# Kernel optimization log

Hardware: AMD Instinct MI355X
Metric: run time of the kernel (lower is better)

## Reference

```python
import jax, jax.numpy as jnp
import numpy as np

N = 50000      # total packed nodes
E = 1600000    # edges (no self loops; layers add them)
G = 64         # graphs in the batch
F_IN = 24      # raw node feature dim
D = 64         # hidden dim
H = 4          # attention heads
C = D // H     # 16 channels per head
L = 3          # GAT layers
NEG = 0.2      # LeakyReLU negative slope (GATv2 default)
EPS = 1e-5     # LayerNorm eps


def setup_inputs() -> dict:
    key = jax.random.key(0)
    ks = jax.random.split(key, 16)
    x = jax.random.normal(ks[0], (N, F_IN), jnp.float32)
    src = jax.random.randint(ks[1], (E,), 0, N)
    dst = jax.random.randint(ks[2], (E,), 0, N)
    dst = jnp.where(dst == src, (dst + 1) % N, dst)  # keep edge list self-loop free
    edge_index = jnp.stack([src, dst]).astype(jnp.int32)
    batch = jnp.sort(jax.random.randint(ks[3], (N,), 0, G)).astype(jnp.int32)
    s = 0.1
    return dict(
        x=x, edge_index=edge_index, batch=batch,
        w_in=jax.random.normal(ks[4], (F_IN, D), jnp.float32) * s,
        b_in=jnp.zeros((D,), jnp.float32),
        w_l=jax.random.normal(ks[5], (L, D, D), jnp.float32) * s,
        b_l=jnp.zeros((L, D), jnp.float32),
        w_r=jax.random.normal(ks[6], (L, D, D), jnp.float32) * s,
        b_r=jnp.zeros((L, D), jnp.float32),
        att=jax.random.normal(ks[7], (L, H, C), jnp.float32) * s,
        b_gat=jnp.zeros((L, D), jnp.float32),
        ln_g=jnp.ones((L, D), jnp.float32),
        ln_b=jnp.zeros((L, D), jnp.float32),
        w_g1=jax.random.normal(ks[8], (D, D // 2), jnp.float32) * s,
        b_g1=jnp.zeros((D // 2,), jnp.float32),
        w_g2=jax.random.normal(ks[9], (D // 2, 1), jnp.float32) * s,
        b_g2=jnp.zeros((1,), jnp.float32),
        w_out=jax.random.normal(ks[10], (D, D), jnp.float32) * s,
        b_out=jnp.zeros((D,), jnp.float32),
    )


def _layernorm(h, g, b):
    m = h.mean(-1, keepdims=True)
    v = ((h - m) ** 2).mean(-1, keepdims=True)
    return (h - m) * jax.lax.rsqrt(v + EPS) * g + b


def _gatv2(h, src, dst, wl, bl, wr, br, att, bg):
    n = h.shape[0]
    xl = (h @ wl + bl).reshape(n, H, C)   # source transform
    xr = (h @ wr + br).reshape(n, H, C)   # target transform
    # edge scores: att . leaky_relu(xl[j] + xr[i])  -> [E', H]
    e = jnp.sum(jax.nn.leaky_relu(xl[src] + xr[dst], NEG) * att, axis=-1)
    emax = jax.ops.segment_max(e, dst, num_segments=n)
    ex = jnp.exp(e - emax[dst])
    denom = jax.ops.segment_sum(ex, dst, num_segments=n)
    alpha = ex / denom[dst]               # segment softmax over incoming edges
    out = jax.ops.segment_sum(alpha[:, :, None] * xl[src], dst, num_segments=n)
    return out.reshape(n, D) + bg


def reference(x, edge_index, batch, w_in, b_in, w_l, b_l, w_r, b_r, att, b_gat,
              ln_g, ln_b, w_g1, b_g1, w_g2, b_g2, w_out, b_out):
    n = x.shape[0]
    loops = jnp.arange(n, dtype=edge_index.dtype)
    src = jnp.concatenate([edge_index[0], loops])  # add self loops once
    dst = jnp.concatenate([edge_index[1], loops])
    h = jax.nn.relu(x @ w_in + b_in)
    for i in range(L):
        res = h
        h = _gatv2(h, src, dst, w_l[i], b_l[i], w_r[i], b_r[i], att[i], b_gat[i])
        h = _layernorm(h + res, ln_g[i], ln_b[i])
        if i < L - 1:
            h = jax.nn.relu(h)
    # GlobalAttention pooling: gate MLP -> per-graph softmax -> weighted sum
    gate = jax.nn.relu(h @ w_g1 + b_g1) @ w_g2 + b_g2  # [N, 1]
    gmax = jax.ops.segment_max(gate, batch, num_segments=G)
    ge = jnp.exp(gate - gmax[batch])
    gs = jax.ops.segment_sum(ge, batch, num_segments=G)
    a = ge / jnp.where(gs > 0, gs, 1.0)[batch]
    emb = jax.ops.segment_sum(a * h, batch, num_segments=G)  # [G, D]
    return jax.nn.relu(emb @ w_out + b_out)
```

## Files before the change

### kernel.cpp

```cpp
#include <hip/hip_runtime.h>

#define NEGS   0.2f
#define LN_EPS 1e-5f
#define BSH    7
#define BN     128
#define TILE   4096
#define LOG2E  1.44269504f

typedef const float* __restrict__ fp;
typedef _Float16 v2h __attribute__((ext_vector_type(2)));
typedef _Float16 v8h __attribute__((ext_vector_type(8)));
typedef float    v4f __attribute__((ext_vector_type(4)));

__device__ __forceinline__ v2h u2h(unsigned u){ union{unsigned u; v2h h;} c; c.u = u; return c.h; }
__device__ __forceinline__ unsigned h2u(v2h h){ union{v2h h; unsigned u;} c; c.h = h; return c.u; }

template<int CTRL>
__device__ __forceinline__ float dppadd(float x){
  int y = __builtin_amdgcn_update_dpp(0, __float_as_int(x), CTRL, 0xF, 0xF, true);
  return x + __int_as_float(y);
}
__device__ __forceinline__ float hsum8(float s){
  s = dppadd<0xB1>(s);
  s = dppadd<0x4E>(s);
  s = dppadd<0x141>(s);
  return s;
}
__device__ __forceinline__ float edge_w(v2h v, v2h xrv, v2h att2, float negm8){
  v2h t = v + xrv;
  t = __builtin_elementwise_max(t, t * (_Float16)NEGS);
  float s = hsum8(__builtin_amdgcn_fdot2(t, att2, negm8, false));
  return __builtin_amdgcn_exp2f(s);
}

__global__ __launch_bounds__(256) void k_in(fp x, fp w, fp b, float* __restrict__ h,
                                            unsigned* __restrict__ h16, int N){
  __shared__ float ws[24*64];
  __shared__ float bs[64];
  __shared__ float xs[4][24];
  int tid = threadIdx.x;
  for (int i = tid; i < 24*64; i += 256) ws[i] = w[i];
  if (tid < 64) bs[tid] = b[tid];
  int r = tid >> 6, c = tid & 63;
  int row = blockIdx.x*4 + r;
  if (c < 24 && row < N) xs[r][c] = x[row*24 + c];
  __syncthreads();
  float acc = bs[c];
  #pragma unroll
  for (int k = 0; k < 24; ++k) acc = fmaf(xs[r][k], ws[k*64 + c], acc);
  float y = fmaxf(acc, 0.f);
  float y1 = __shfl_down(y, 1);
  if (row < N){
    h[(size_t)row*64 + c] = y;
    if (!(c & 1)){
      v2h p; p.x = (_Float16)y; p.y = (_Float16)y1;
      h16[(size_t)row*32 + (c >> 1)] = h2u(p);
    }
  }
}

__global__ __launch_bounds__(256) void k_wprep(fp w_l, fp w_r, _Float16* __restrict__ wf){
  int lm = blockIdx.x;
  const float* src = ((lm & 1) ? w_r : w_l) + (lm >> 1)*4096;
  _Float16* dst = wf + lm*4096;
  for (int d = threadIdx.x; d < 4096; d += 256){
    int j = d & 7, l = (d >> 3) & 63, kc = (d >> 9) & 1, nt = d >> 10;
    int k = kc*32 + (l >> 4)*8 + j;
    int n = nt*16 + (l & 15);
    dst[d] = (_Float16)src[k*64 + n];
  }
}

__global__ __launch_bounds__(256) void t_hist(const int* __restrict__ dstA, int* __restrict__ counts,
                                              int E, int K, int ntiles){
  __shared__ int hist[512];
  int t = blockIdx.x, tid = threadIdx.x;
  for (int i = tid; i < K; i += 256) hist[i] = 0;
  __syncthreads();
  int e0 = t*TILE, e1 = min(e0 + TILE, E);
  for (int e = e0 + tid; e < e1; e += 256)
    atomicAdd(&hist[dstA[e] >> BSH], 1);
  __syncthreads();
  for (int i = tid; i < K; i += 256) counts[i*ntiles + t] = hist[i];
}

__global__ __launch_bounds__(512) void s_scan_tiles(int* __restrict__ counts, int* __restrict__ btotal,
                                                    int ntiles){
  __shared__ int s[512];
  int b = blockIdx.x, tid = threadIdx.x;
  int v = (tid < ntiles) ? counts[b*ntiles + tid] : 0;
  s[tid] = v;
  __syncthreads();
  for (int off = 1; off < 512; off <<= 1){
    int t = (tid >= off) ? s[tid - off] : 0;
    __syncthreads();
    s[tid] += t;
    __syncthreads();
  }
  if (tid < ntiles) counts[b*ntiles + tid] = s[tid] - v;
  if (tid == 511) btotal[b] = s[511];
}

__global__ __launch_bounds__(512) void s_scan_buckets(const int* __restrict__ btotal,
                                                      int* __restrict__ bbase, int K, int E){
  __shared__ int s[512];
  int tid = threadIdx.x;
  int v = (tid < K) ? btotal[tid] : 0;
  s[tid] = v;
  __syncthreads();
  for (int off = 1; off < 512; off <<= 1){
    int t = (tid >= off) ? s[tid - off] : 0;
    __syncthreads();
    s[tid] += t;
    __syncthreads();
  }
  if (tid < K) bbase[tid] = s[tid] - v;
  if (tid == 0) bbase[K] = E;
}

__global__ __launch_bounds__(256) void t_scatter(const int* __restrict__ srcA, const int* __restrict__ dstA,
                                                 const int* __restrict__ counts, const int* __restrict__ bbase,
                                                 unsigned* __restrict__ packed, int E, int K, int ntiles){
  __shared__ int gb[512];
  __shared__ int cur[512];
  int t = blockIdx.x, tid = threadIdx.x;
  for (int i = tid; i < K; i += 256){
    gb[i] = bbase[i] + counts[i*ntiles + t];
    cur[i] = 0;
  }
  __syncthreads();
  int e0 = t*TILE, e1 = min(e0 + TILE, E);
  for (int e = e0 + tid; e < e1; e += 256){
    int d = dstA[e], sv = srcA[e];
    int b = d >> BSH;
    int p = atomicAdd(&cur[b], 1);
    packed[gb[b] + p] = ((unsigned)(d & (BN-1)) << 25) | (unsigned)sv;
  }
}

__global__ __launch_bounds__(256) void k_fine(const unsigned* __restrict__ packed, const int* __restrict__ bbase,
                                              int* __restrict__ row_ptr, int* __restrict__ col, int N, int K){
  __shared__ int hist[BN];
  __shared__ int excl[BN];
  int b = blockIdx.x, tid = threadIdx.x;
  int node0 = b << BSH;
  int e_base = bbase[b], e_end = bbase[b+1];
  if (tid < BN) hist[tid] = 0;
  __syncthreads();
  for (int e = e_base + tid; e < e_end; e += 256)
    atomicAdd(&hist[packed[e] >> 25], 1);
  __syncthreads();
  int v = (tid < BN) ? hist[tid] : 0;
  if (tid < BN) excl[tid] = v;
  __syncthreads();
  for (int off = 1; off < BN; off <<= 1){
    int t2 = 0;
    if (tid < BN && tid >= off) t2 = excl[tid - off];
    __syncthreads();
    if (tid < BN) excl[tid] += t2;
    __syncthreads();
  }
  int nn = min(BN, N - node0);
  if (tid < nn) row_ptr[node0 + tid] = e_base + excl[tid] - v;
  if (b == K-1 && tid == 0) row_ptr[N] = e_end;
  if (tid < BN) hist[tid] = excl[tid] - v;
  __syncthreads();
  for (int e = e_base + tid; e < e_end; e += 256){
    unsigned u = packed[e];
    int dl = u >> 25;
    int p = atomicAdd(&hist[dl], 1);
    col[e_base + p] = (int)(u & 0x1FFFFFFu);
  }
}

__global__ __launch_bounds__(256) void k_xfm(const unsigned* __restrict__ h16,
                                             const _Float16* __restrict__ wf,
                                             fp blg, fp brg,
                                             unsigned* __restrict__ xl16, unsigned* __restrict__ xr16, int N){
  int tid = threadIdx.x, wave = tid >> 6, lane = tid & 63;
  int quad = lane >> 4, ln = lane & 15;
  int m0 = blockIdx.x*64 + wave*16;
  if (m0 >= N) return;
  int m = m0 + ln;
  bool mv = m < N;
  v8h a0 = {}, a1 = {};
  if (mv){
    a0 = *(const v8h*)&h16[(size_t)m*32 + quad*4];
    a1 = *(const v8h*)&h16[(size_t)m*32 + 16 + quad*4];
  }
  #pragma unroll
  for (int mat = 0; mat < 2; ++mat){
    const _Float16* wb = wf + mat*4096;
    fp bias = mat ? brg : blg;
    unsigned* dst = mat ? xr16 : xl16;
    #pragma unroll
    for (int nt = 0; nt < 4; ++nt){
      v8h b0 = *(const v8h*)&wb[nt*1024 + lane*8];
      v8h b1 = *(const v8h*)&wb[nt*1024 + 512 + lane*8];
      float bv = bias[nt*16 + ln];
      v4f acc = {bv, bv, bv, bv};
      acc = __builtin_amdgcn_mfma_f32_16x16x32_f16(a0, b0, acc, 0, 0, 0);
      acc = __builtin_amdgcn_mfma_f32_16x16x32_f16(a1, b1, acc, 0, 0, 0);
      #pragma unroll
      for (int r = 0; r < 4; ++r){
        float partner = __shfl_xor(acc[r], 1);
        int node = m0 + quad*4 + r;
        if (!(lane & 1) && node < N){
          v2h p; p.x = (_Float16)acc[r]; p.y = (_Float16)partner;
          dst[(size_t)node*32 + nt*8 + (ln >> 1)] = h2u(p);
        }
      }
    }
  }
}

__global__ __launch_bounds__(256) void k_gat(const unsigned* __restrict__ xl16, const unsigned* __restrict__ xr16,
                                             float* __restrict__ h, unsigned* __restrict__ h16,
                                             const int* __restrict__ row_ptr, const int* __restrict__ col,
                                             fp att, fp bg, fp lng, fp lnb, int N, int do_relu){
  int lane = threadIdx.x & 63;
  int node = blockIdx.x*4 + (threadIdx.x >> 6);
  if (node >= N) return;
  int l = lane & 31;
  bool lower = lane < 32;
  int off = lower ? 0 : 1;
  v2h att2; att2.x = (_Float16)(att[2*l] * LOG2E); att2.y = (_Float16)(att[2*l+1] * LOG2E);
  v2h xrv = u2h(xr16[(size_t)node*32 + l]);
  v2h xlv = u2h(xl16[(size_t)node*32 + l]);
  v2h ts = xlv + xrv;
  ts = __builtin_elementwise_max(ts, ts * (_Float16)NEGS);
  const float m = hsum8(__builtin_amdgcn_fdot2(ts, att2, 0.f, false));
  const float negm8 = m * -0.125f;
  float den0 = lower ? 1.f : 0.f, den1 = 0.f, den2 = 0.f, den3 = 0.f;
  float a0x = lower ? (float)xlv.x : 0.f, a0y = lower ? (float)xlv.y : 0.f;
  float a1x = 0.f, a1y = 0.f, a2x = 0.f, a2y = 0.f, a3x = 0.f, a3y = 0.f;
  int e = row_ptr[node], e1 = row_ptr[node+1];
  for (; e + 16 <= e1; e += 16){
    int j0 = col[e+off],    j1 = col[e+2+off],  j2 = col[e+4+off],  j3 = col[e+6+off];
    int j4 = col[e+8+off],  j5 = col[e+10+off], j6 = col[e+12+off], j7 = col[e+14+off];
    v2h v0 = u2h(xl16[(size_t)j0*32 + l]);
    v2h v1 = u2h(xl16[(size_t)j1*32 + l]);
    v2h v2 = u2h(xl16[(size_t)j2*32 + l]);
    v2h v3 = u2h(xl16[(size_t)j3*32 + l]);
    v2h v4 = u2h(xl16[(size_t)j4*32 + l]);
    v2h v5 = u2h(xl16[(size_t)j5*32 + l]);
    v2h v6 = u2h(xl16[(size_t)j6*32 + l]);
    v2h v7 = u2h(xl16[(size_t)j7*32 + l]);
    float w0 = edge_w(v0, xrv, att2, negm8);
    float w1 = edge_w(v1, xrv, att2, negm8);
    float w2 = edge_w(v2, xrv, att2, negm8);
    float w3 = edge_w(v3, xrv, att2, negm8);
    float w4 = edge_w(v4, xrv, att2, negm8);
    float w5 = edge_w(v5, xrv, att2, negm8);
    float w6 = edge_w(v6, xrv, att2, negm8);
    float w7 = edge_w(v7, xrv, att2, negm8);
    den0 += w0; a0x = fmaf(w0, (float)v0.x, a0x); a0y = fmaf(w0, (float)v0.y, a0y);
    den1 += w1; a1x = fmaf(w1, (float)v1.x, a1x); a1y = fmaf(w1, (float)v1.y, a1y);
    den2 += w2; a2x = fmaf(w2, (float)v2.x, a2x); a2y = fmaf(w2, (float)v2.y, a2y);
    den3 += w3; a3x = fmaf(w3, (float)v3.x, a3x); a3y = fmaf(w3, (float)v3.y, a3y);
    den0 += w4; a0x = fmaf(w4, (float)v4.x, a0x); a0y = fmaf(w4, (float)v4.y, a0y);
    den1 += w5; a1x = fmaf(w5, (float)v5.x, a1x); a1y = fmaf(w5, (float)v5.y, a1y);
    den2 += w6; a2x = fmaf(w6, (float)v6.x, a2x); a2y = fmaf(w6, (float)v6.y, a2y);
    den3 += w7; a3x = fmaf(w7, (float)v7.x, a3x); a3y = fmaf(w7, (float)v7.y, a3y);
  }
  for (; e + 8 <= e1; e += 8){
    int j0 = col[e+off], j1 = col[e+2+off], j2 = col[e+4+off], j3 = col[e+6+off];
    v2h v0 = u2h(xl16[(size_t)j0*32 + l]);
    v2h v1 = u2h(xl16[(size_t)j1*32 + l]);
    v2h v2 = u2h(xl16[(size_t)j2*32 + l]);
    v2h v3 = u2h(xl16[(size_t)j3*32 + l]);
    float w0 = edge_w(v0, xrv, att2, negm8);
    float w1 = edge_w(v1, xrv, att2, negm8);
    float w2 = edge_w(v2, xrv, att2, negm8);
    float w3 = edge_w(v3, xrv, att2, negm8);
    den0 += w0; a0x = fmaf(w0, (float)v0.x, a0x); a0y = fmaf(w0, (float)v0.y, a0y);
    den1 += w1; a1x = fmaf(w1, (float)v1.x, a1x); a1y = fmaf(w1, (float)v1.y, a1y);
    den2 += w2; a2x = fmaf(w2, (float)v2.x, a2x); a2y = fmaf(w2, (float)v2.y, a2y);
    den3 += w3; a3x = fmaf(w3, (float)v3.x, a3x); a3y = fmaf(w3, (float)v3.y, a3y);
  }
  for (; e + 2 <= e1; e += 2){
    int j0 = col[e+off];
    v2h v0 = u2h(xl16[(size_t)j0*32 + l]);
    float w0 = edge_w(v0, xrv, att2, negm8);
    den0 += w0; a0x = fmaf(w0, (float)v0.x, a0x); a0y = fmaf(w0, (float)v0.y, a0y);
  }
  if (e < e1){
    int j0 = col[e];
    v2h v0 = u2h(xl16[(size_t)j0*32 + l]);
    float w0 = edge_w(v0, xrv, att2, negm8);
    if (!lower) w0 = 0.f;
    den0 += w0; a0x = fmaf(w0, (float)v0.x, a0x); a0y = fmaf(w0, (float)v0.y, a0y);
  }
  float den = (den0 + den1) + (den2 + den3);
  float ax = (a0x + a1x) + (a2x + a3x);
  float ay = (a0y + a1y) + (a2y + a3y);
  den += __shfl_xor(den, 32);
  ax  += __shfl_xor(ax, 32);
  ay  += __shfl_xor(ay, 32);
  float inv = 1.f / den;
  float2 bg2 = *(const float2*)&bg[2*l];
  float2 h2  = *(const float2*)&h[(size_t)node*64 + 2*l];
  float ox = ax*inv + bg2.x + h2.x;
  float oy = ay*inv + bg2.y + h2.y;
  float sl = ox + oy;
  #pragma unroll
  for (int o = 1; o < 32; o <<= 1) sl += __shfl_xor(sl, o);
  float mean = sl * (1.f/64.f);
  float dx = ox - mean, dy = oy - mean;
  float vsl = dx*dx + dy*dy;
  #pragma unroll
  for (int o = 1; o < 32; o <<= 1) vsl += __shfl_xor(vsl, o);
  float rs = rsqrtf(vsl * (1.f/64.f) + LN_EPS);
  float2 lg2 = *(const float2*)&lng[2*l];
  float2 lb2 = *(const float2*)&lnb[2*l];
  float yx = dx*rs*lg2.x + lb2.x;
  float yy = dy*rs*lg2.y + lb2.y;
  if (do_relu){ yx = fmaxf(yx, 0.f); yy = fmaxf(yy, 0.f); }
  if (lower){
    float2 y2; y2.x = yx; y2.y = yy;
    *(float2*)&h[(size_t)node*64 + 2*l] = y2;
    v2h p; p.x = (_Float16)yx; p.y = (_Float16)yy;
    h16[(size_t)node*32 + l] = h2u(p);
  }
}

__global__ __launch_bounds__(256) void k_gate(const float* __restrict__ h, fp w1, fp b1, fp w2, fp b2,
                                              float* __restrict__ gate, int N){
  __shared__ float w1s[2048];
  __shared__ float hrow[16][64];
  int tid = threadIdx.x;
  for (int i = tid*4; i < 2048; i += 1024) *(float4*)&w1s[i] = *(const float4*)&w1[i];
  int base = blockIdx.x*16;
  int nrows = min(16, N - base);
  int lim = nrows*64;
  for (int i = tid*4; i < lim; i += 1024)
    *(float4*)&hrow[0][i] = *(const float4*)&h[(size_t)base*64 + i];
  __syncthreads();
  int wave = tid >> 6, lane = tid & 63;
  int j = lane & 31, half = lane >> 5;
  float b1v = b1[j], w2v = w2[j], b2v = b2[0];
  int k0 = half*32;
  #pragma unroll
  for (int it = 0; it < 4; ++it){
    int r = wave*4 + it;
    int node = base + r;
    if (node >= N) break;
    float s = 0.f;
    #pragma unroll 8
    for (int k = k0; k < k0 + 32; ++k) s = fmaf(hrow[r][k], w1s[k*32 + j], s);
    s += __shfl_xor(s, 32);
    float hid = fmaxf(s + b1v, 0.f);
    float contrib = (half == 0) ? hid * w2v : 0.f;
    #pragma unroll
    for (int o = 1; o < 64; o <<= 1) contrib += __shfl_xor(contrib, o);
    if (lane == 0) gate[node] = contrib + b2v;
  }
}

__global__ __launch_bounds__(256) void k_gmax(const float* __restrict__ gate, const int* __restrict__ batch,
                                              float* __restrict__ gmax, float* __restrict__ gsum,
                                              float* __restrict__ embsum, int N){
  int g = blockIdx.x, tid = threadIdx.x;
  if (tid < 64) embsum[g*64 + tid] = 0.f;
  if (tid == 64) gsum[g] = 0.f;
  int lo = 0, hi = N;
  while (lo < hi){ int mid = (lo + hi) >> 1; if (batch[mid] < g) lo = mid + 1; else hi = mid; }
  int start = lo;
  hi = N;
  while (lo < hi){ int mid = (lo + hi) >> 1; if (batch[mid] < g + 1) lo = mid + 1; else hi = mid; }
  int end = lo;
  float m = -3.4e38f;
  for (int i = start + tid; i < end; i += 256) m = fmaxf(m, gate[i]);
  #pragma unroll
  for (int o = 1; o < 64; o <<= 1) m = fmaxf(m, __shfl_xor(m, o));
  __shared__ float ws[4];
  if ((tid & 63) == 0) ws[tid >> 6] = m;
  __syncthreads();
  if (tid == 0) gmax[g] = fmaxf(fmaxf(ws[0], ws[1]), fmaxf(ws[2], ws[3]));
}

__global__ __launch_bounds__(256) void k_emb(const float* __restrict__ h, const float* __restrict__ gate,
                                             const int* __restrict__ batch, const float* __restrict__ gmax,
                                             float* __restrict__ gsum, float* __restrict__ embsum, int N){
  int lane = threadIdx.x & 63;
  int wv = blockIdx.x*4 + (threadIdx.x >> 6);
  int s = wv*64;
  if (s >= N) return;
  int e = min(s + 64, N);
  int cur = batch[s];
  float gm = gmax[cur];
  float acc = 0.f, asum = 0.f;
  for (int i = s; i < e; ++i){
    int g = batch[i];
    if (g != cur){
      atomicAdd(&embsum[cur*64 + lane], acc);
      if (lane == 0) atomicAdd(&gsum[cur], asum);
      acc = 0.f; asum = 0.f; cur = g; gm = gmax[g];
    }
    float a = __expf(gate[i] - gm);
    acc = fmaf(a, h[(size_t)i*64 + lane], acc);
    asum += a;
  }
  atomicAdd(&embsum[cur*64 + lane], acc);
  if (lane == 0) atomicAdd(&gsum[cur], asum);
}

__global__ __launch_bounds__(64) void k_out(const float* __restrict__ embsum, const float* __restrict__ gsum,
                                            fp w_out, fp b_out, float* __restrict__ out, int G){
  int g = blockIdx.x, lane = threadIdx.x;
  __shared__ float emb[64];
  float gs = gsum[g];
  float inv = (gs > 0.f) ? 1.f/gs : 1.f;
  emb[lane] = embsum[g*64 + lane] * inv;
  __syncthreads();
  float o2 = b_out[lane];
  #pragma unroll 8
  for (int d = 0; d < 64; ++d) o2 = fmaf(emb[d], w_out[d*64 + lane], o2);
  out[g*64 + lane] = fmaxf(o2, 0.f);
}

extern "C" void kernel_launch(void* const* d_in, const int* in_sizes, int n_in,
                              void* d_out, int out_size, void* d_ws, size_t ws_size,
                              hipStream_t stream) {
  const int N = in_sizes[0] / 24;
  const int E = in_sizes[1] / 2;
  const int G = out_size / 64;
  const int K = (N + BN - 1) >> BSH;
  const int ntiles = (E + TILE - 1) / TILE;

  fp x      = (fp)d_in[0];
  const int* edge  = (const int*)d_in[1];
  const int* batch = (const int*)d_in[2];
  fp w_in   = (fp)d_in[3];
  fp b_in   = (fp)d_in[4];
  fp w_l    = (fp)d_in[5];
  fp b_l    = (fp)d_in[6];
  fp w_r    = (fp)d_in[7];
  fp b_r    = (fp)d_in[8];
  fp att    = (fp)d_in[9];
  fp b_gat  = (fp)d_in[10];
  fp ln_g   = (fp)d_in[11];
  fp ln_b   = (fp)d_in[12];
  fp w_g1   = (fp)d_in[13];
  fp b_g1   = (fp)d_in[14];
  fp w_g2   = (fp)d_in[15];
  fp b_g2   = (fp)d_in[16];
  fp w_out  = (fp)d_in[17];
  fp b_out  = (fp)d_in[18];
  float* out = (float*)d_out;

  char* wp = (char*)d_ws;
  auto alloc = [&](size_t bytes) -> char* {
    char* p = wp; wp += (bytes + 255) & ~(size_t)255; return p;
  };
  float*    h       = (float*)    alloc((size_t)N*64*sizeof(float));
  unsigned* h16     = (unsigned*) alloc((size_t)N*32*sizeof(unsigned));
  unsigned* xl16    = (unsigned*) alloc((size_t)N*32*sizeof(unsigned));
  unsigned* xr16    = (unsigned*) alloc((size_t)N*32*sizeof(unsigned));
  int*      col     = (int*)      alloc((size_t)E*sizeof(int));
  unsigned* packed  = (unsigned*) alloc((size_t)E*sizeof(unsigned));
  int*      counts  = (int*)      alloc((size_t)K*ntiles*sizeof(int));
  int*      btotal  = (int*)      alloc((size_t)K*sizeof(int));
  int*      bbase   = (int*)      alloc((size_t)(K+1)*sizeof(int));
  int*      row_ptr = (int*)      alloc((size_t)(N+1)*sizeof(int));
  float*    gate    = (float*)    alloc((size_t)N*sizeof(float));
  float*    gmax    = (float*)    alloc((size_t)G*sizeof(float));
  float*    gsum    = (float*)    alloc((size_t)(G + G*64)*sizeof(float));
  float*    embsum  = gsum + G;
  _Float16* wf      = (_Float16*) alloc((size_t)3*2*4096*sizeof(_Float16));

  const int* srcA = edge;
  const int* dstA = edge + E;

  k_in<<<(N + 3)/4, 256, 0, stream>>>(x, w_in, b_in, h, h16, N);
  k_wprep<<<6, 256, 0, stream>>>(w_l, w_r, wf);

  t_hist<<<ntiles, 256, 0, stream>>>(dstA, counts, E, K, ntiles);
  s_scan_tiles<<<K, 512, 0, stream>>>(counts, btotal, ntiles);
  s_scan_buckets<<<1, 512, 0, stream>>>(btotal, bbase, K, E);
  t_scatter<<<ntiles, 256, 0, stream>>>(srcA, dstA, counts, bbase, packed, E, K, ntiles);
  k_fine<<<K, 256, 0, stream>>>(packed, bbase, row_ptr, col, N, K);

  for (int i = 0; i < 3; ++i){
    k_xfm<<<(N + 63)/64, 256, 0, stream>>>(h16, wf + i*8192, b_l + i*64, b_r + i*64,
                                           xl16, xr16, N);
    k_gat<<<(N + 3)/4, 256, 0, stream>>>(xl16, xr16, h, h16, row_ptr, col,
                                         att + i*64, b_gat + i*64, ln_g + i*64, ln_b + i*64,
                                         N, i < 2 ? 1 : 0);
  }
  k_gate<<<(N + 15)/16, 256, 0, stream>>>(h, w_g1, b_g1, w_g2, b_g2, gate, N);
  k_gmax<<<G, 256, 0, stream>>>(gate, batch, gmax, gsum, embsum, N);
  k_emb<<<(N + 255)/256, 256, 0, stream>>>(h, gate, batch, gmax, gsum, embsum, N);
  k_out<<<G, 64, 0, stream>>>(embsum, gsum, w_out, b_out, out, G);
}
```

Measured before the change: 383.8 us.

## Merge setup kernels, use last-block scan, vectorize col loads, read fp16 in pooling

Merges the input projection, edge histogram, counter reset and weight-prep kernels into one launch, and folds the bucket scan into the tile scan using a last-block atomic counter. This cuts the number of kernel launches and the serialization between them. The GAT aggregation now peels edges until the index is 4-aligned and loads column indices with int4 vector loads instead of scalar loads. Pooling reads the fp16 copy of h instead of fp32, halving that traffic but adding rounding error relative to the fp32 reference; the last-block pattern relies on threadfence ordering being correct.

```diff
diff --git a/kernel.cpp b/kernel.cpp
--- a/kernel.cpp
+++ b/kernel.cpp
@@ -33,60 +33,66 @@
   return __builtin_amdgcn_exp2f(s);
 }
 
-__global__ __launch_bounds__(256) void k_in(fp x, fp w, fp b, float* __restrict__ h,
-                                            unsigned* __restrict__ h16, int N){
-  __shared__ float ws[24*64];
-  __shared__ float bs[64];
-  __shared__ float xs[4][24];
-  int tid = threadIdx.x;
-  for (int i = tid; i < 24*64; i += 256) ws[i] = w[i];
-  if (tid < 64) bs[tid] = b[tid];
-  int r = tid >> 6, c = tid & 63;
-  int row = blockIdx.x*4 + r;
-  if (c < 24 && row < N) xs[r][c] = x[row*24 + c];
-  __syncthreads();
-  float acc = bs[c];
-  #pragma unroll
-  for (int k = 0; k < 24; ++k) acc = fmaf(xs[r][k], ws[k*64 + c], acc);
-  float y = fmaxf(acc, 0.f);
-  float y1 = __shfl_down(y, 1);
-  if (row < N){
-    h[(size_t)row*64 + c] = y;
-    if (!(c & 1)){
-      v2h p; p.x = (_Float16)y; p.y = (_Float16)y1;
-      h16[(size_t)row*32 + (c >> 1)] = h2u(p);
+__global__ __launch_bounds__(256) void f_in_hist(fp x, fp w, fp b, float* __restrict__ h,
+                                                 unsigned* __restrict__ h16,
+                                                 const int* __restrict__ dstA, int* __restrict__ counts,
+                                                 int* __restrict__ ctr,
+                                                 fp w_l, fp w_r, _Float16* __restrict__ wf,
+                                                 int N, int E, int K, int ntiles, int NB_IN){
+  __shared__ __align__(16) float sm[1700];
+  int bid = blockIdx.x, tid = threadIdx.x;
+  if (bid < NB_IN){
+    float* ws = sm;
+    float* bs = sm + 1536;
+    float* xs = sm + 1600;
+    for (int i = tid; i < 1536; i += 256) ws[i] = w[i];
+    if (tid < 64) bs[tid] = b[tid];
+    int r = tid >> 6, c = tid & 63;
+    int row = bid*4 + r;
+    if (c < 24 && row < N) xs[r*24 + c] = x[row*24 + c];
+    __syncthreads();
+    float acc = bs[c];
+    #pragma unroll
+    for (int k = 0; k < 24; ++k) acc = fmaf(xs[r*24 + k], ws[k*64 + c], acc);
+    float y = fmaxf(acc, 0.f);
+    float y1 = __shfl_down(y, 1);
+    if (row < N){
+      h[(size_t)row*64 + c] = y;
+      if (!(c & 1)){
+        v2h p; p.x = (_Float16)y; p.y = (_Float16)y1;
+        h16[(size_t)row*32 + (c >> 1)] = h2u(p);
+      }
     }
-  }
-}
-
-__global__ __launch_bounds__(256) void k_wprep(fp w_l, fp w_r, _Float16* __restrict__ wf){
-  int lm = blockIdx.x;
-  const float* src = ((lm & 1) ? w_r : w_l) + (lm >> 1)*4096;
-  _Float16* dst = wf + lm*4096;
-  for (int d = threadIdx.x; d < 4096; d += 256){
-    int j = d & 7, l = (d >> 3) & 63, kc = (d >> 9) & 1, nt = d >> 10;
-    int k = kc*32 + (l >> 4)*8 + j;
-    int n = nt*16 + (l & 15);
-    dst[d] = (_Float16)src[k*64 + n];
-  }
-}
-
-__global__ __launch_bounds__(256) void t_hist(const int* __restrict__ dstA, int* __restrict__ counts,
-                                              int E, int K, int ntiles){
-  __shared__ int hist[512];
-  int t = blockIdx.x, tid = threadIdx.x;
-  for (int i = tid; i < K; i += 256) hist[i] = 0;
-  __syncthreads();
-  int e0 = t*TILE, e1 = min(e0 + TILE, E);
-  for (int e = e0 + tid; e < e1; e += 256)
-    atomicAdd(&hist[dstA[e] >> BSH], 1);
-  __syncthreads();
-  for (int i = tid; i < K; i += 256) counts[i*ntiles + t] = hist[i];
-}
-
-__global__ __launch_bounds__(512) void s_scan_tiles(int* __restrict__ counts, int* __restrict__ btotal,
-                                                    int ntiles){
+  } else if (bid < NB_IN + ntiles){
+    int* hist = (int*)sm;
+    int t = bid - NB_IN;
+    for (int i = tid; i < K; i += 256) hist[i] = 0;
+    __syncthreads();
+    int e0 = t*TILE, e1 = min(e0 + TILE, E);
+    for (int e = e0 + tid; e < e1; e += 256)
+      atomicAdd(&hist[dstA[e] >> BSH], 1);
+    __syncthreads();
+    for (int i = tid; i < K; i += 256) counts[i*ntiles + t] = hist[i];
+  } else if (bid == NB_IN + ntiles){
+    if (tid == 0) ctr[0] = 0;
+  } else {
+    int lm = bid - NB_IN - ntiles - 1;
+    const float* src = ((lm & 1) ? w_r : w_l) + (lm >> 1)*4096;
+    _Float16* dst = wf + lm*4096;
+    for (int d = tid; d < 4096; d += 256){
+      int j = d & 7, l = (d >> 3) & 63, kc = (d >> 9) & 1, nt = d >> 10;
+      int k = kc*32 + (l >> 4)*8 + j;
+      int n = nt*16 + (l & 15);
+      dst[d] = (_Float16)src[k*64 + n];
+    }
+  }
+}
+
+__global__ __launch_bounds__(512) void s_scan(int* __restrict__ counts, int* __restrict__ btotal,
+                                              int* __restrict__ bbase, int* __restrict__ ctr,
+                                              int K, int E, int ntiles){
   __shared__ int s[512];
+  __shared__ int isLast;
   int b = blockIdx.x, tid = threadIdx.x;
   int v = (tid < ntiles) ? counts[b*ntiles + tid] : 0;
   s[tid] = v;
@@ -99,14 +105,14 @@
   }
   if (tid < ntiles) counts[b*ntiles + tid] = s[tid] - v;
   if (tid == 511) btotal[b] = s[511];
-}
-
-__global__ __launch_bounds__(512) void s_scan_buckets(const int* __restrict__ btotal,
-                                                      int* __restrict__ bbase, int K, int E){
-  __shared__ int s[512];
-  int tid = threadIdx.x;
-  int v = (tid < K) ? btotal[tid] : 0;
-  s[tid] = v;
+  __threadfence();
+  __syncthreads();
+  if (tid == 0){ int old = atomicAdd(ctr, 1); isLast = (old == (int)gridDim.x - 1) ? 1 : 0; }
+  __syncthreads();
+  if (!isLast) return;
+  __threadfence();
+  int v2 = (tid < K) ? btotal[tid] : 0;
+  s[tid] = v2;
   __syncthreads();
   for (int off = 1; off < 512; off <<= 1){
     int t = (tid >= off) ? s[tid - off] : 0;
@@ -114,7 +120,7 @@
     s[tid] += t;
     __syncthreads();
   }
-  if (tid < K) bbase[tid] = s[tid] - v;
+  if (tid < K) bbase[tid] = s[tid] - v2;
   if (tid == 0) bbase[K] = E;
 }
 
@@ -235,9 +241,27 @@
   float a0x = lower ? (float)xlv.x : 0.f, a0y = lower ? (float)xlv.y : 0.f;
   float a1x = 0.f, a1y = 0.f, a2x = 0.f, a2y = 0.f, a3x = 0.f, a3y = 0.f;
   int e = row_ptr[node], e1 = row_ptr[node+1];
+  while ((e & 3) && e < e1){
+    int j0 = col[e];
+    v2h v0 = u2h(xl16[(size_t)j0*32 + l]);
+    float w0 = edge_w(v0, xrv, att2, negm8);
+    if (!lower) w0 = 0.f;
+    den0 += w0; a0x = fmaf(w0, (float)v0.x, a0x); a0y = fmaf(w0, (float)v0.y, a0y);
+    ++e;
+  }
   for (; e + 16 <= e1; e += 16){
-    int j0 = col[e+off],    j1 = col[e+2+off],  j2 = col[e+4+off],  j3 = col[e+6+off];
-    int j4 = col[e+8+off],  j5 = col[e+10+off], j6 = col[e+12+off], j7 = col[e+14+off];
+    int4 c0 = *(const int4*)&col[e];
+    int4 c1 = *(const int4*)&col[e+4];
+    int4 c2 = *(const int4*)&col[e+8];
+    int4 c3 = *(const int4*)&col[e+12];
+    int j0 = lower ? c0.x : c0.y;
+    int j1 = lower ? c0.z : c0.w;
+    int j2 = lower ? c1.x : c1.y;
+    int j3 = lower ? c1.z : c1.w;
+    int j4 = lower ? c2.x : c2.y;
+    int j5 = lower ? c2.z : c2.w;
+    int j6 = lower ? c3.x : c3.y;
+    int j7 = lower ? c3.z : c3.w;
     v2h v0 = u2h(xl16[(size_t)j0*32 + l]);
     v2h v1 = u2h(xl16[(size_t)j1*32 + l]);
     v2h v2 = u2h(xl16[(size_t)j2*32 + l]);
@@ -264,7 +288,12 @@
     den3 += w7; a3x = fmaf(w7, (float)v7.x, a3x); a3y = fmaf(w7, (float)v7.y, a3y);
   }
   for (; e + 8 <= e1; e += 8){
-    int j0 = col[e+off], j1 = col[e+2+off], j2 = col[e+4+off], j3 = col[e+6+off];
+    int4 c0 = *(const int4*)&col[e];
+    int4 c1 = *(const int4*)&col[e+4];
+    int j0 = lower ? c0.x : c0.y;
+    int j1 = lower ? c0.z : c0.w;
+    int j2 = lower ? c1.x : c1.y;
+    int j3 = lower ? c1.z : c1.w;
     v2h v0 = u2h(xl16[(size_t)j0*32 + l]);
     v2h v1 = u2h(xl16[(size_t)j1*32 + l]);
     v2h v2 = u2h(xl16[(size_t)j2*32 + l]);
@@ -379,10 +408,11 @@
   if (tid == 0) gmax[g] = fmaxf(fmaxf(ws[0], ws[1]), fmaxf(ws[2], ws[3]));
 }
 
-__global__ __launch_bounds__(256) void k_emb(const float* __restrict__ h, const float* __restrict__ gate,
+__global__ __launch_bounds__(256) void k_emb(const unsigned* __restrict__ h16, const float* __restrict__ gate,
                                              const int* __restrict__ batch, const float* __restrict__ gmax,
                                              float* __restrict__ gsum, float* __restrict__ embsum, int N){
   int lane = threadIdx.x & 63;
+  int half = lane & 1, li = lane >> 1;
   int wv = blockIdx.x*4 + (threadIdx.x >> 6);
   int s = wv*64;
   if (s >= N) return;
@@ -398,7 +428,9 @@
       acc = 0.f; asum = 0.f; cur = g; gm = gmax[g];
     }
     float a = __expf(gate[i] - gm);
-    acc = fmaf(a, h[(size_t)i*64 + lane], acc);
+    v2h p = u2h(h16[(size_t)i*32 + li]);
+    float hv = half ? (float)p.y : (float)p.x;
+    acc = fmaf(a, hv, acc);
     asum += a;
   }
   atomicAdd(&embsum[cur*64 + lane], acc);
@@ -427,6 +459,7 @@
   const int G = out_size / 64;
   const int K = (N + BN - 1) >> BSH;
   const int ntiles = (E + TILE - 1) / TILE;
+  const int NB_IN = (N + 3) / 4;
 
   fp x      = (fp)d_in[0];
   const int* edge  = (const int*)d_in[1];
@@ -468,16 +501,14 @@
   float*    gsum    = (float*)    alloc((size_t)(G + G*64)*sizeof(float));
   float*    embsum  = gsum + G;
   _Float16* wf      = (_Float16*) alloc((size_t)3*2*4096*sizeof(_Float16));
+  int*      ctr     = (int*)      alloc(256);
 
   const int* srcA = edge;
   const int* dstA = edge + E;
 
-  k_in<<<(N + 3)/4, 256, 0, stream>>>(x, w_in, b_in, h, h16, N);
-  k_wprep<<<6, 256, 0, stream>>>(w_l, w_r, wf);
-
-  t_hist<<<ntiles, 256, 0, stream>>>(dstA, counts, E, K, ntiles);
-  s_scan_tiles<<<K, 512, 0, stream>>>(counts, btotal, ntiles);
-  s_scan_buckets<<<1, 512, 0, stream>>>(btotal, bbase, K, E);
+  f_in_hist<<<NB_IN + ntiles + 7, 256, 0, stream>>>(x, w_in, b_in, h, h16, dstA, counts,
+                                                    ctr, w_l, w_r, wf, N, E, K, ntiles, NB_IN);
+  s_scan<<<K, 512, 0, stream>>>(counts, btotal, bbase, ctr, K, E, ntiles);
   t_scatter<<<ntiles, 256, 0, stream>>>(srcA, dstA, counts, bbase, packed, E, K, ntiles);
   k_fine<<<K, 256, 0, stream>>>(packed, bbase, row_ptr, col, N, K);
 
@@ -490,6 +521,6 @@
   }
   k_gate<<<(N + 15)/16, 256, 0, stream>>>(h, w_g1, b_g1, w_g2, b_g2, gate, N);
   k_gmax<<<G, 256, 0, stream>>>(gate, batch, gmax, gsum, embsum, N);
-  k_emb<<<(N + 255)/256, 256, 0, stream>>>(h, gate, batch, gmax, gsum, embsum, N);
+  k_emb<<<(N + 255)/256, 256, 0, stream>>>(h16, gate, batch, gmax, gsum, embsum, N);
   k_out<<<G, 64, 0, stream>>>(embsum, gsum, w_out, b_out, out, G);
 }
```

Result: slower. 451.3 us (+17.6%).
